# Optimization experiments

Measured on AMD Instinct MI355X. Metric: run time of the kernel, lower is better.

The kernel has to match this reference:

```python
import jax, jax.numpy as jnp
import numpy as np


def _gcn_layer(x, W, b, src, dst, norm, n_nodes):
    # x: [N, Fin]; transform first (PyG GCNConv): h = x @ W
    h = x @ W  # [N, Fout]
    # gather-scale-scatter: out[d] += norm_e * h[s] over edges (incl. self loops)
    msgs = h[src] * norm[:, None]  # [E+N, Fout]
    agg = jax.ops.segment_sum(msgs, dst, num_segments=n_nodes)
    return agg + b


def setup_inputs() -> dict:
    key = jax.random.key(0)
    k1, k2, k3, k4 = jax.random.split(key, 4)
    N, E, F_IN, HID, OUT = 50000, 800000, 128, 256, 128
    x = jax.random.normal(k1, (N, F_IN), dtype=jnp.float32)
    edge_index = jax.random.randint(k2, (2, E), 0, N, dtype=jnp.int64)
    W1 = jax.random.normal(k3, (F_IN, HID), dtype=jnp.float32) / np.sqrt(F_IN)
    b1 = jnp.zeros((HID,), dtype=jnp.float32)
    W2 = jax.random.normal(k4, (HID, OUT), dtype=jnp.float32) / np.sqrt(HID)
    b2 = jnp.zeros((OUT,), dtype=jnp.float32)
    return {"x": x, "edge_index": edge_index, "W1": W1, "b1": b1, "W2": W2, "b2": b2}


def reference(x, edge_index, W1, b1, W2, b2):
    N = x.shape[0]
    # GCN normalization with self loops: A_hat = D^-1/2 (A + I) D^-1/2
    self_loops = jnp.arange(N, dtype=edge_index.dtype)
    src = jnp.concatenate([edge_index[0], self_loops])
    dst = jnp.concatenate([edge_index[1], self_loops])
    deg = jax.ops.segment_sum(jnp.ones_like(dst, dtype=x.dtype), dst, num_segments=N)
    dinv = jnp.where(deg > 0, jax.lax.rsqrt(deg), 0.0)
    norm = dinv[src] * dinv[dst]  # [E+N]
    h = _gcn_layer(x, W1, b1, src, dst, norm, N)
    h = jax.nn.relu(h)  # dropout is identity in eval mode
    out = _gcn_layer(h, W2, b2, src, dst, norm, N)
    return out  # unsupervised mode returns raw embeddings [N, 128]
```

## Files before the change

kernel.cpp:

```cpp
#include <hip/hip_runtime.h>
#include <hip/hip_bf16.h>


static constexpr int N_NODES = 50000;
static constexpr int N_EDGES = 800000;
static constexpr int F_IN = 128;
static constexpr int HID  = 256;
static constexpr int F_OUT = 128;
static constexpr int H2P  = HID + 8;

typedef __attribute__((ext_vector_type(8))) short short8;
typedef __attribute__((ext_vector_type(4))) float f32x4;

__device__ __forceinline__ unsigned short f2bf(float f) {
    union { float f; unsigned u; } x; x.f = f;
    unsigned r = x.u + 0x7FFF + ((x.u >> 16) & 1);
    return (unsigned short)(r >> 16);
}
__device__ __forceinline__ float bf2f(unsigned short h) {
    union { unsigned u; float f; } x; x.u = ((unsigned)h) << 16;
    return x.f;
}

__global__ void deg_wt_kernel(const int* __restrict__ dst, int* __restrict__ deg,
                              int* __restrict__ pos, int E,
                              const float* __restrict__ W1, unsigned short* __restrict__ w1t,
                              const float* __restrict__ W2, unsigned short* __restrict__ w2t,
                              int EB, int NB1) {
    const int b = blockIdx.x;
    if (b < EB) {
        int i = b * 256 + threadIdx.x;
        if (i < E) pos[i] = atomicAdd(&deg[dst[i]], 1);
    } else if (b < EB + NB1) {
        int t = (b - EB) * 256 + threadIdx.x;
        if (t < F_IN * HID) {
            int n = t / F_IN, k = t - n * F_IN;
            w1t[t] = f2bf(W1[(size_t)k * HID + n]);
        }
    } else {
        int t = (b - EB - NB1) * 256 + threadIdx.x;
        if (t < HID * F_OUT) {
            int n = t / HID, k = t - n * HID;
            w2t[t] = f2bf(W2[(size_t)k * F_OUT + n]);
        }
    }
}

__global__ __launch_bounds__(256) void scan_reduce_dinv(const int* __restrict__ deg,
                                                        int* __restrict__ bsums,
                                                        float* __restrict__ dinv, int N) {
    int i = blockIdx.x * 256 + threadIdx.x;
    int v = (i < N) ? deg[i] : 0;
    if (i < N) dinv[i] = rsqrtf((float)(v + 1));
#pragma unroll
    for (int ofs = 32; ofs > 0; ofs >>= 1) v += __shfl_down(v, ofs);
    __shared__ int ws[4];
    if ((threadIdx.x & 63) == 0) ws[threadIdx.x >> 6] = v;
    __syncthreads();
    if (threadIdx.x == 0) bsums[blockIdx.x] = ws[0] + ws[1] + ws[2] + ws[3];
}

__global__ __launch_bounds__(256) void scan_final_scalex(const int* __restrict__ deg,
                                                         const int* __restrict__ bsums,
                                                         int* __restrict__ off, int N, int nb,
                                                         const float* __restrict__ x,
                                                         const float* __restrict__ dinv,
                                                         unsigned short* __restrict__ xs) {
    const int tid = threadIdx.x;
    if ((int)blockIdx.x >= nb) {
        int i = (blockIdx.x - nb) * 256 + tid;
        if (i < N_NODES * F_IN / 8) {
            float dv = dinv[i >> 4];
            float4 v0 = ((const float4*)x)[i * 2];
            float4 v1 = ((const float4*)x)[i * 2 + 1];
            short8 o;
            o[0] = (short)f2bf(v0.x * dv); o[1] = (short)f2bf(v0.y * dv);
            o[2] = (short)f2bf(v0.z * dv); o[3] = (short)f2bf(v0.w * dv);
            o[4] = (short)f2bf(v1.x * dv); o[5] = (short)f2bf(v1.y * dv);
            o[6] = (short)f2bf(v1.z * dv); o[7] = (short)f2bf(v1.w * dv);
            *(short8*)(xs + (size_t)i * 8) = o;
        }
        return;
    }
    __shared__ int bs[256];
    __shared__ int s[256];
    bs[tid] = (tid < nb) ? bsums[tid] : 0;
    const int i = blockIdx.x * 256 + tid;
    int v = (i < N) ? deg[i] : 0;
    s[tid] = v;
    __syncthreads();
    for (int ofs = 1; ofs < 256; ofs <<= 1) {
        int tb = (tid >= ofs) ? bs[tid - ofs] : 0;
        int tv = (tid >= ofs) ? s[tid - ofs] : 0;
        __syncthreads();
        bs[tid] += tb;
        s[tid] += tv;
        __syncthreads();
    }
    int bbase = (blockIdx.x == 0) ? 0 : bs[blockIdx.x - 1];
    int excl = (tid == 0) ? 0 : s[tid - 1];
    if (i <= N) off[i] = bbase + excl;
}

__global__ void scatter_kernel(const int* __restrict__ src, const int* __restrict__ dst,
                               const int* __restrict__ pos, const int* __restrict__ off,
                               int* __restrict__ csr, int E) {
    int i = blockIdx.x * blockDim.x + threadIdx.x;
    if (i < E) csr[off[dst[i]] + pos[i]] = src[i];
}

template <int MODE>
__global__ __launch_bounds__(256) void agg_bf16(const unsigned short* __restrict__ hs,
                                                const int* __restrict__ off,
                                                const int* __restrict__ csr,
                                                const float* __restrict__ dinv,
                                                const float* __restrict__ bias,
                                                void* __restrict__ outp, int N) {
    const int wid = threadIdx.x >> 6;
    const int n = blockIdx.x * 4 + wid;
    if (n >= N) return;
    const int lane = threadIdx.x & 63;
    const int lane16 = lane & 15;
    const int slot = lane >> 4;

    float va[8], vb[8], vc[8], vd[8];
#pragma unroll
    for (int j = 0; j < 8; j++) { va[j] = 0.f; vb[j] = 0.f; vc[j] = 0.f; vd[j] = 0.f; }

    if (slot == 0) {
        short8 s = *(const short8*)(hs + (size_t)n * 128 + lane16 * 8);
#pragma unroll
        for (int j = 0; j < 8; j++) va[j] = bf2f((unsigned short)s[j]);
    }

    const int e0 = off[n];
    const int e1 = off[n + 1];
    for (int e = e0 + slot; e < e1; e += 16) {
        const int i1 = e + 4, i2 = e + 8, i3 = e + 12;
        const float f1 = (i1 < e1) ? 1.f : 0.f;
        const float f2 = (i2 < e1) ? 1.f : 0.f;
        const float f3 = (i3 < e1) ? 1.f : 0.f;
        const int c1 = min(i1, e1 - 1), c2 = min(i2, e1 - 1), c3 = min(i3, e1 - 1);
        int s0 = csr[e];
        int s1 = csr[c1];
        int s2 = csr[c2];
        int s3 = csr[c3];
        short8 v0 = *(const short8*)(hs + (size_t)s0 * 128 + lane16 * 8);
        short8 v1 = *(const short8*)(hs + (size_t)s1 * 128 + lane16 * 8);
        short8 v2 = *(const short8*)(hs + (size_t)s2 * 128 + lane16 * 8);
        short8 v3 = *(const short8*)(hs + (size_t)s3 * 128 + lane16 * 8);
#pragma unroll
        for (int j = 0; j < 8; j++) va[j] += bf2f((unsigned short)v0[j]);
#pragma unroll
        for (int j = 0; j < 8; j++) vb[j] = fmaf(f1, bf2f((unsigned short)v1[j]), vb[j]);
#pragma unroll
        for (int j = 0; j < 8; j++) vc[j] = fmaf(f2, bf2f((unsigned short)v2[j]), vc[j]);
#pragma unroll
        for (int j = 0; j < 8; j++) vd[j] = fmaf(f3, bf2f((unsigned short)v3[j]), vd[j]);
    }
#pragma unroll
    for (int j = 0; j < 8; j++) va[j] += vb[j] + vc[j] + vd[j];

#pragma unroll
    for (int j = 0; j < 8; j++) va[j] += __shfl_down(va[j], 32);
#pragma unroll
    for (int j = 0; j < 8; j++) va[j] += __shfl_down(va[j], 16);

    if (lane < 16) {
        float dv = dinv[n];
        if (MODE == 0) {
            short8 o;
#pragma unroll
            for (int j = 0; j < 8; j++) o[j] = (short)f2bf(va[j] * dv);
            *(short8*)((unsigned short*)outp + (size_t)n * 128 + lane * 8) = o;
        } else {
            float* op = (float*)outp + (size_t)n * 128 + lane * 8;
            float4 o0, o1;
            o0.x = va[0] * dv + bias[lane * 8 + 0];
            o0.y = va[1] * dv + bias[lane * 8 + 1];
            o0.z = va[2] * dv + bias[lane * 8 + 2];
            o0.w = va[3] * dv + bias[lane * 8 + 3];
            o1.x = va[4] * dv + bias[lane * 8 + 4];
            o1.y = va[5] * dv + bias[lane * 8 + 5];
            o1.z = va[6] * dv + bias[lane * 8 + 6];
            o1.w = va[7] * dv + bias[lane * 8 + 7];
            ((float4*)op)[0] = o0;
            ((float4*)op)[1] = o1;
        }
    }
}

__global__ __launch_bounds__(256) void gemm12(const unsigned short* __restrict__ Y,
                                              const unsigned short* __restrict__ w1t,
                                              const float* __restrict__ b1,
                                              const unsigned short* __restrict__ w2t,
                                              const float* __restrict__ dinv,
                                              unsigned short* __restrict__ hs2, int M) {
    __shared__ unsigned short h2s[32 * H2P];

    const int wid = threadIdx.x >> 6;
    const int lane = threadIdx.x & 63;
    const int an = lane & 15;
    const int q = lane >> 4;
    const int rowgrp = wid & 1;
    const int colgrp = wid >> 1;
    const int m0 = blockIdx.x * 32 + rowgrp * 16;
    const int lrow0 = rowgrp * 16;

    {
        short8 a[4];
        {
            int row = m0 + an;
            if (row >= M) row = M - 1;
            const unsigned short* xp = Y + (size_t)row * F_IN + q * 8;
#pragma unroll
            for (int c = 0; c < 4; c++) a[c] = *(const short8*)(xp + c * 32);
        }
#pragma unroll
        for (int t = 0; t < 8; t++) {
            const int col = (colgrp * 8 + t) * 16 + an;
            const unsigned short* wp = w1t + (size_t)col * F_IN + q * 8;
            short8 b[4];
#pragma unroll
            for (int c = 0; c < 4; c++) b[c] = *(const short8*)(wp + c * 32);
            f32x4 acc = {0.f, 0.f, 0.f, 0.f};
#pragma unroll
            for (int c = 0; c < 4; c++)
                acc = __builtin_amdgcn_mfma_f32_16x16x32_bf16(a[c], b[c], acc, 0, 0, 0);
            const float bv = b1[col];
#pragma unroll
            for (int rr = 0; rr < 4; rr++)
                h2s[(lrow0 + q * 4 + rr) * H2P + col] = f2bf(fmaxf(acc[rr] + bv, 0.f));
        }
    }
    __syncthreads();

    {
        short8 a[8];
        {
            const unsigned short* hp = &h2s[(lrow0 + an) * H2P + q * 8];
#pragma unroll
            for (int c = 0; c < 8; c++) a[c] = *(const short8*)(hp + c * 32);
        }
        float dv[4];
#pragma unroll
        for (int rr = 0; rr < 4; rr++) {
            int m = m0 + q * 4 + rr;
            dv[rr] = (m < M) ? dinv[m] : 0.f;
        }
#pragma unroll
        for (int t = 0; t < 4; t++) {
            const int col = colgrp * 64 + t * 16 + an;
            const unsigned short* wp = w2t + (size_t)col * HID + q * 8;
            short8 b[8];
#pragma unroll
            for (int c = 0; c < 8; c++) b[c] = *(const short8*)(wp + c * 32);
            f32x4 acc = {0.f, 0.f, 0.f, 0.f};
#pragma unroll
            for (int c = 0; c < 8; c++)
                acc = __builtin_amdgcn_mfma_f32_16x16x32_bf16(a[c], b[c], acc, 0, 0, 0);
#pragma unroll
            for (int rr = 0; rr < 4; rr++) {
                int m = m0 + q * 4 + rr;
                if (m < M) hs2[(size_t)m * F_OUT + col] = f2bf(acc[rr] * dv[rr]);
            }
        }
    }
}

extern "C" void kernel_launch(void* const* d_in, const int* in_sizes, int n_in,
                              void* d_out, int out_size, void* d_ws, size_t ws_size,
                              hipStream_t stream) {
    const float* x  = (const float*)d_in[0];
    const int*   ei = (const int*)d_in[1];
    const float* W1 = (const float*)d_in[2];
    const float* b1 = (const float*)d_in[3];
    const float* W2 = (const float*)d_in[4];
    const float* b2 = (const float*)d_in[5];

    const int N = N_NODES;
    const int E = N_EDGES;
    const int* srcp = ei;
    const int* dstp = ei + E;

    char* base = (char*)d_ws;
    size_t o = 0;
    auto alloc = [&](size_t bytes) {
        void* p = base + o;
        o = (o + bytes + 255) & ~(size_t)255;
        return p;
    };
    int*            deg  = (int*)alloc((size_t)N * 4);
    int*            offs = (int*)alloc((size_t)(N + 1) * 4);
    float*          dinv = (float*)alloc((size_t)N * 4);
    int*            bsum = (int*)alloc(256 * 4);
    int*            pos  = (int*)alloc((size_t)E * 4);
    int*            csr  = (int*)alloc((size_t)E * 4);
    unsigned short* xs   = (unsigned short*)alloc((size_t)N * F_IN * 2);
    unsigned short* Y    = (unsigned short*)alloc((size_t)N * F_IN * 2);
    unsigned short* w1t  = (unsigned short*)alloc((size_t)F_IN * HID * 2);
    unsigned short* w2t  = (unsigned short*)alloc((size_t)HID * F_OUT * 2);
    unsigned short* hs2  = xs;

    hipMemsetAsync(deg, 0, (size_t)N * 4, stream);

    const int NB  = (N + 256) / 256;
    const int NBX = (N * F_IN / 8 + 255) / 256;
    const int EB  = (E + 255) / 256;
    const int NB1 = (F_IN * HID + 255) / 256;
    const int NB2 = (HID * F_OUT + 255) / 256;

    deg_wt_kernel<<<EB + NB1 + NB2, 256, 0, stream>>>(dstp, deg, pos, E, W1, w1t, W2, w2t, EB, NB1);
    scan_reduce_dinv<<<NB, 256, 0, stream>>>(deg, bsum, dinv, N);
    scan_final_scalex<<<NB + NBX, 256, 0, stream>>>(deg, bsum, offs, N, NB, x, dinv, xs);
    scatter_kernel<<<EB, 256, 0, stream>>>(srcp, dstp, pos, offs, csr, E);

    agg_bf16<0><<<(N + 3) / 4, 256, 0, stream>>>(xs, offs, csr, dinv, nullptr, Y, N);
    gemm12<<<(N + 31) / 32, 256, 0, stream>>>(Y, w1t, b1, w2t, dinv, hs2, N);
    agg_bf16<1><<<(N + 3) / 4, 256, 0, stream>>>(hs2, offs, csr, dinv, b2, d_out, N);
}
```

Baseline: 267.9 us.

## Make fused GEMM persistent with register-resident weight fragments

Rewrites the fused two-layer GEMM as a persistent kernel of 512 blocks with 512 threads. Each wave loads its slices of W1 and W2 into registers once, then loops over 16-row tiles, so weights are no longer reloaded for every tile. The LDS row padding also changes to reduce bank conflicts. The kernel assumes M is a multiple of 16, which holds for N=50000, and adds two barriers per tile.

```diff
diff --git a/kernel.cpp b/kernel.cpp
--- a/kernel.cpp
+++ b/kernel.cpp
@@ -7,7 +7,7 @@
 static constexpr int F_IN = 128;
 static constexpr int HID  = 256;
 static constexpr int F_OUT = 128;
-static constexpr int H2P  = HID + 8;
+static constexpr int H2P  = 258;
 
 typedef __attribute__((ext_vector_type(8))) short short8;
 typedef __attribute__((ext_vector_type(4))) float f32x4;
@@ -190,81 +190,82 @@
     }
 }
 
-__global__ __launch_bounds__(256) void gemm12(const unsigned short* __restrict__ Y,
-                                              const unsigned short* __restrict__ w1t,
-                                              const float* __restrict__ b1,
-                                              const unsigned short* __restrict__ w2t,
-                                              const float* __restrict__ dinv,
-                                              unsigned short* __restrict__ hs2, int M) {
-    __shared__ unsigned short h2s[32 * H2P];
+__global__ __launch_bounds__(512, 4) void gemm12(const unsigned short* __restrict__ Y,
+                                                 const unsigned short* __restrict__ w1t,
+                                                 const float* __restrict__ b1,
+                                                 const unsigned short* __restrict__ w2t,
+                                                 const float* __restrict__ dinv,
+                                                 unsigned short* __restrict__ hs2, int M) {
+    __shared__ unsigned short h2s[16 * H2P];
 
     const int wid = threadIdx.x >> 6;
     const int lane = threadIdx.x & 63;
     const int an = lane & 15;
     const int q = lane >> 4;
-    const int rowgrp = wid & 1;
-    const int colgrp = wid >> 1;
-    const int m0 = blockIdx.x * 32 + rowgrp * 16;
-    const int lrow0 = rowgrp * 16;
-
+
+    short8 b1f[2][4];
+    float bv[2];
+#pragma unroll
+    for (int t = 0; t < 2; t++) {
+        const int col = wid * 32 + t * 16 + an;
+        const unsigned short* wp = w1t + (size_t)col * F_IN + q * 8;
+#pragma unroll
+        for (int c = 0; c < 4; c++) b1f[t][c] = *(const short8*)(wp + c * 32);
+        bv[t] = b1[col];
+    }
+    short8 b2f[8];
+    const int colB = wid * 16 + an;
     {
+        const unsigned short* wp = w2t + (size_t)colB * HID + q * 8;
+#pragma unroll
+        for (int c = 0; c < 8; c++) b2f[c] = *(const short8*)(wp + c * 32);
+    }
+
+    const int T = M >> 4;
+    for (int t0 = blockIdx.x; t0 < T; t0 += gridDim.x) {
+        const int m0 = t0 * 16;
+
         short8 a[4];
         {
-            int row = m0 + an;
-            if (row >= M) row = M - 1;
-            const unsigned short* xp = Y + (size_t)row * F_IN + q * 8;
-#pragma unroll
-            for (int c = 0; c < 4; c++) a[c] = *(const short8*)(xp + c * 32);
-        }
-#pragma unroll
-        for (int t = 0; t < 8; t++) {
-            const int col = (colgrp * 8 + t) * 16 + an;
-            const unsigned short* wp = w1t + (size_t)col * F_IN + q * 8;
-            short8 b[4];
-#pragma unroll
-            for (int c = 0; c < 4; c++) b[c] = *(const short8*)(wp + c * 32);
+            const unsigned short* yp = Y + (size_t)(m0 + an) * F_IN + q * 8;
+#pragma unroll
+            for (int c = 0; c < 4; c++) a[c] = *(const short8*)(yp + c * 32);
+        }
+        f32x4 accA0 = {0.f, 0.f, 0.f, 0.f};
+        f32x4 accA1 = {0.f, 0.f, 0.f, 0.f};
+#pragma unroll
+        for (int c = 0; c < 4; c++) {
+            accA0 = __builtin_amdgcn_mfma_f32_16x16x32_bf16(a[c], b1f[0][c], accA0, 0, 0, 0);
+            accA1 = __builtin_amdgcn_mfma_f32_16x16x32_bf16(a[c], b1f[1][c], accA1, 0, 0, 0);
+        }
+        {
+            const int c0 = wid * 32 + an;
+            unsigned short* hrow = &h2s[(q * 4) * H2P];
+#pragma unroll
+            for (int rr = 0; rr < 4; rr++) {
+                hrow[rr * H2P + c0]      = f2bf(fmaxf(accA0[rr] + bv[0], 0.f));
+                hrow[rr * H2P + c0 + 16] = f2bf(fmaxf(accA1[rr] + bv[1], 0.f));
+            }
+        }
+        __syncthreads();
+
+        {
+            short8 h[8];
+            const unsigned short* hp = &h2s[an * H2P + q * 8];
+#pragma unroll
+            for (int c = 0; c < 8; c++) h[c] = *(const short8*)(hp + c * 32);
             f32x4 acc = {0.f, 0.f, 0.f, 0.f};
 #pragma unroll
-            for (int c = 0; c < 4; c++)
-                acc = __builtin_amdgcn_mfma_f32_16x16x32_bf16(a[c], b[c], acc, 0, 0, 0);
-            const float bv = b1[col];
-#pragma unroll
-            for (int rr = 0; rr < 4; rr++)
-                h2s[(lrow0 + q * 4 + rr) * H2P + col] = f2bf(fmaxf(acc[rr] + bv, 0.f));
-        }
-    }
-    __syncthreads();
-
-    {
-        short8 a[8];
-        {
-            const unsigned short* hp = &h2s[(lrow0 + an) * H2P + q * 8];
-#pragma unroll
-            for (int c = 0; c < 8; c++) a[c] = *(const short8*)(hp + c * 32);
-        }
-        float dv[4];
-#pragma unroll
-        for (int rr = 0; rr < 4; rr++) {
-            int m = m0 + q * 4 + rr;
-            dv[rr] = (m < M) ? dinv[m] : 0.f;
-        }
-#pragma unroll
-        for (int t = 0; t < 4; t++) {
-            const int col = colgrp * 64 + t * 16 + an;
-            const unsigned short* wp = w2t + (size_t)col * HID + q * 8;
-            short8 b[8];
-#pragma unroll
-            for (int c = 0; c < 8; c++) b[c] = *(const short8*)(wp + c * 32);
-            f32x4 acc = {0.f, 0.f, 0.f, 0.f};
-#pragma unroll
             for (int c = 0; c < 8; c++)
-                acc = __builtin_amdgcn_mfma_f32_16x16x32_bf16(a[c], b[c], acc, 0, 0, 0);
-#pragma unroll
-            for (int rr = 0; rr < 4; rr++) {
-                int m = m0 + q * 4 + rr;
-                if (m < M) hs2[(size_t)m * F_OUT + col] = f2bf(acc[rr] * dv[rr]);
-            }
-        }
+                acc = __builtin_amdgcn_mfma_f32_16x16x32_bf16(h[c], b2f[c], acc, 0, 0, 0);
+            const float4 dv4 = ((const float4*)dinv)[(m0 >> 2) + q];
+            unsigned short* op = hs2 + (size_t)(m0 + q * 4) * F_OUT + colB;
+            op[0]         = f2bf(acc[0] * dv4.x);
+            op[F_OUT]     = f2bf(acc[1] * dv4.y);
+            op[2 * F_OUT] = f2bf(acc[2] * dv4.z);
+            op[3 * F_OUT] = f2bf(acc[3] * dv4.w);
+        }
+        __syncthreads();
     }
 }
 
@@ -316,6 +317,6 @@
     scatter_kernel<<<EB, 256, 0, stream>>>(srcp, dstp, pos, offs, csr, E);
 
     agg_bf16<0><<<(N + 3) / 4, 256, 0, stream>>>(xs, offs, csr, dinv, nullptr, Y, N);
-    gemm12<<<(N + 31) / 32, 256, 0, stream>>>(Y, w1t, b1, w2t, dinv, hs2, N);
+    gemm12<<<512, 512, 0, stream>>>(Y, w1t, b1, w2t, dinv, hs2, N);
     agg_bf16<1><<<(N + 3) / 4, 256, 0, stream>>>(hs2, offs, csr, dinv, b2, d_out, N);
 }
```

Result: faster. 250.7 us (-6.4%).
